# Kernel tuning notes

Measured on AMD Instinct MI355X. Metric: run time of the kernel, lower is better.

The kernel has to match this reference:

```python
import jax, jax.numpy as jnp
import numpy as np

H = 3072; NH = 24; HD = 128; MLP_D = 12288
B = 1; IMG = 1536; REF = 512; TXT = 256

def _gelu_tanh(x):
    return jax.nn.gelu(x, approximate=True)

def _ln(x, eps=1e-6):
    m = jnp.mean(x, axis=-1, keepdims=True)
    v = jnp.var(x, axis=-1, keepdims=True)
    return (x - m) * jax.lax.rsqrt(v + eps)

def _rms(x, g, eps=1e-6):
    return x * jax.lax.rsqrt(jnp.mean(x * x, axis=-1, keepdims=True) + eps) * g

def _rot_half(x):
    # interleaved rotate-half: (x0,x1,x2,x3,...) -> (-x1,x0,-x3,x2,...)
    x2 = x.reshape(x.shape[:-1] + (-1, 2))
    return jnp.stack([-x2[..., 1], x2[..., 0]], axis=-1).reshape(x.shape)

def setup_inputs():
    key = jax.random.key(0)
    ks = jax.random.split(key, 16)
    s = 0.02
    # rope tables for image tokens (interleaved layout, values repeated x2)
    inv_freq = 1.0 / (10000.0 ** (jnp.arange(0, HD // 2, dtype=jnp.float32) / (HD // 2)))
    ang = jnp.arange(IMG, dtype=jnp.float32)[:, None] * inv_freq[None, :]   # [IMG, HD//2]
    ang = jnp.repeat(ang, 2, axis=-1)                                       # [IMG, HD]
    return {
        'x':   jax.random.normal(ks[0], (B, IMG + TXT, H), jnp.float32),
        'vec': jax.random.normal(ks[1], (B, H), jnp.float32),
        'ref': jax.random.normal(ks[2], (B, REF, H), jnp.float32),
        'cos': jnp.cos(ang), 'sin': jnp.sin(ang),
        'mod_w':  jax.random.normal(ks[3], (H, 3 * H), jnp.float32) * s,
        'mod_b':  jnp.zeros((3 * H,), jnp.float32),
        'rf1_w':  jax.random.normal(ks[4], (H, H), jnp.float32) * s,
        'rf1_b':  jnp.zeros((H,), jnp.float32),
        'rf2_w':  jax.random.normal(ks[5], (H, H), jnp.float32) * s,
        'rf2_b':  jnp.zeros((H,), jnp.float32),
        'rln_g':  jnp.ones((H,), jnp.float32),
        'rln_b':  jnp.zeros((H,), jnp.float32),
        'lin1_w': jax.random.normal(ks[6], (H, 3 * H + MLP_D), jnp.float32) * s,
        'lin1_b': jnp.zeros((3 * H + MLP_D,), jnp.float32),
        'q_g':    jnp.ones((HD,), jnp.float32),
        'k_g':    jnp.ones((HD,), jnp.float32),
        'lin2_w': jax.random.normal(ks[7], (H + MLP_D, H), jnp.float32) * s,
        'lin2_b': jnp.zeros((H,), jnp.float32),
        'text_mask': jnp.ones((B, TXT), jnp.int32),
        'img_len': IMG, 'txt_len': TXT,
    }

def _forward(x, vec, ref, cos, sin, mod_w, mod_b, rf1_w, rf1_b, rf2_w, rf2_b,
             rln_g, rln_b, lin1_w, lin1_b, q_g, k_g, lin2_w, lin2_b,
             text_mask, img_len, txt_len):
    Bb = x.shape[0]
    ref_len = ref.shape[1]
    # modulation (ModulateDiT: SiLU -> Linear -> chunk(3))
    mod = jnp.dot(jax.nn.silu(vec), mod_w) + mod_b
    shift, scale, gate = jnp.split(mod, 3, axis=-1)
    x_mod = _ln(x) * (1.0 + scale[:, None]) + shift[:, None]
    # ref MLP + affine LayerNorm
    r = jnp.dot(_gelu_tanh(jnp.dot(ref, rf1_w) + rf1_b), rf2_w) + rf2_b
    r = _ln(r) * rln_g + rln_b
    # token reassembly: [img | ref | txt]
    xc = jnp.concatenate([x_mod[:, :img_len], r, x_mod[:, img_len:]], axis=1)
    h = jnp.dot(xc, lin1_w) + lin1_b
    qkv, mlp = h[..., :3 * H], h[..., 3 * H:]
    L2 = xc.shape[1]
    q, k, v = [t.reshape(Bb, L2, NH, HD) for t in jnp.split(qkv, 3, axis=-1)]
    # q drops the ref span; ref contributes K/V only
    q = jnp.concatenate([q[:, :img_len], q[:, img_len + ref_len:]], axis=1)
    q = _rms(q, q_g)
    k = _rms(k, k_g)
    # rotary only on image tokens
    c = cos[None, :, None, :]; s = sin[None, :, None, :]
    img_q = q[:, :img_len] * c + _rot_half(q[:, :img_len]) * s
    img_k = k[:, :img_len] * c + _rot_half(k[:, :img_len]) * s
    q = jnp.concatenate([img_q, q[:, img_len:]], axis=1)          # [B, Lq, NH, HD]
    k = jnp.concatenate([img_k, k[:, img_len:]], axis=1)          # [B, Lkv, NH, HD]
    # varlen mask (cu_seqlens semantics): valid attends valid, pad attends pad
    tmask = text_mask.astype(bool)
    qv  = jnp.concatenate([jnp.ones((Bb, img_len), bool), tmask], axis=1)
    kvv = jnp.concatenate([jnp.ones((Bb, img_len + ref_len), bool), tmask], axis=1)
    allowed = (qv[:, None, :, None] == kvv[:, None, None, :])     # [B,1,Lq,Lkv]
    scores = jnp.einsum('bqhd,bkhd->bhqk', q, k) * (HD ** -0.5)
    scores = jnp.where(allowed, scores, jnp.asarray(-1e9, scores.dtype))
    p = jax.nn.softmax(scores, axis=-1)
    attn = jnp.einsum('bhqk,bkhd->bqhd', p, v).reshape(Bb, img_len + txt_len, H)
    mlp = jnp.concatenate([mlp[:, :img_len], mlp[:, img_len + ref_len:]], axis=1)
    out = jnp.dot(jnp.concatenate([attn, _gelu_tanh(mlp)], axis=-1), lin2_w) + lin2_b
    return x + out * gate[:, None]

def reference(x, vec, ref, cos, sin, mod_w, mod_b, rf1_w, rf1_b, rf2_w, rf2_b,
              rln_g, rln_b, lin1_w, lin1_b, q_g, k_g, lin2_w, lin2_b,
              text_mask, img_len, txt_len):
    return _forward(x, vec, ref, cos, sin, mod_w, mod_b, rf1_w, rf1_b, rf2_w, rf2_b,
                    rln_g, rln_b, lin1_w, lin1_b, q_g, k_g, lin2_w, lin2_b,
                    text_mask, img_len, txt_len)
```

## Files before the change

kernel.cpp:

```cpp
#include <hip/hip_runtime.h>
#include <cstdint>
#include <cstddef>

typedef unsigned short u16;
typedef unsigned int   u32;
typedef __bf16 bf16_t;
typedef bf16_t bf16x8 __attribute__((ext_vector_type(8)));
typedef float  f32x4  __attribute__((ext_vector_type(4)));
typedef u16    u16x4  __attribute__((ext_vector_type(4)));


__device__ __forceinline__ float b2f(u16 b){ u32 u=((u32)b)<<16; float f; __builtin_memcpy(&f,&u,4); return f; }
__device__ __forceinline__ u16 f2b(float f){ u32 u; __builtin_memcpy(&u,&f,4); u = u + 0x7fffu + ((u>>16)&1u); return (u16)(u>>16); }
__device__ __forceinline__ float gelu_f(float x){
  float x3 = x*x*x;
  return 0.5f*x*(1.f + tanhf(0.7978845608028654f*(x + 0.044715f*x3)));
}

__device__ __forceinline__ void gload_lds16(const void* g, void* l){
  __builtin_amdgcn_global_load_lds((const __attribute__((address_space(1))) void*)g,
                                   (__attribute__((address_space(3))) void*)l, 16, 0, 0);
}

template<int NW, bool MX>
__device__ __forceinline__ float bred(float v, float* red){
  #pragma unroll
  for (int o=32;o;o>>=1){ float u=__shfl_down(v,o,64); v = MX? fmaxf(v,u) : v+u; }
  const int t = threadIdx.x;
  if ((t&63)==0) red[t>>6]=v;
  __syncthreads();
  float r = red[0];
  #pragma unroll
  for (int i=1;i<NW;i++) r = MX? fmaxf(r,red[i]) : r+red[i];
  __syncthreads();
  return r;
}

__device__ __forceinline__ void unpack8(uint4 u, float* f){
  f[0]=b2f((u16)(u.x&0xffffu)); f[1]=b2f((u16)(u.x>>16));
  f[2]=b2f((u16)(u.y&0xffffu)); f[3]=b2f((u16)(u.y>>16));
  f[4]=b2f((u16)(u.z&0xffffu)); f[5]=b2f((u16)(u.z>>16));
  f[6]=b2f((u16)(u.w&0xffffu)); f[7]=b2f((u16)(u.w>>16));
}

__global__ void modv_part(const float* __restrict__ vec, const float* __restrict__ W,
                          float* __restrict__ part){
  __shared__ float s[128];
  const int t = threadIdx.x;
  const int j = blockIdx.x*256 + t;
  const int i0 = blockIdx.y*128;
  if (t < 128){ float v = vec[i0+t]; s[t] = v/(1.f+__expf(-v)); }
  __syncthreads();
  float acc = 0.f;
  #pragma unroll 8
  for (int i=0;i<128;i++) acc += s[i]*W[(size_t)(i0+i)*9216 + j];
  part[(size_t)blockIdx.y*9216 + j] = acc;
}
__global__ void modv_reduce(const float* __restrict__ part, const float* __restrict__ mb,
                            float* __restrict__ modp){
  const int j = blockIdx.x*256 + threadIdx.x;
  float a = mb[j];
  #pragma unroll
  for (int c=0;c<24;c++) a += part[(size_t)c*9216 + j];
  modp[j] = a;
}

__global__ void convT(const float* __restrict__ W, u16* __restrict__ Wt, int Kd, int Nd){
  __shared__ float Ls[32][33];
  const int tx = threadIdx.x, ty = threadIdx.y;
  const int n0 = blockIdx.x*32, k0 = blockIdx.y*32;
  #pragma unroll
  for (int r=0;r<4;r++) Ls[ty+r*8][tx] = W[(size_t)(k0+ty+r*8)*Nd + n0+tx];
  __syncthreads();
  #pragma unroll
  for (int r=0;r<4;r++) Wt[(size_t)(n0+ty+r*8)*Kd + k0+tx] = f2b(Ls[tx][ty+r*8]);
}

__global__ void convertF2B(const float* __restrict__ src, u16* __restrict__ dst){
  const size_t i = ((size_t)blockIdx.x*256 + threadIdx.x)*4;
  const float4 v = *(const float4*)(src+i);
  u16x4 o; o.x=f2b(v.x); o.y=f2b(v.y); o.z=f2b(v.z); o.w=f2b(v.w);
  *(u16x4*)(dst+i) = o;
}

__global__ void ln_modulate(const float* __restrict__ x, const float* __restrict__ modp,
                            u16* __restrict__ xc){
  __shared__ float red[4];
  const int row = blockIdx.x, t = threadIdx.x;
  const float* xr = x + (size_t)row*3072;
  float4 v[3]; float s=0.f, ss=0.f;
  #pragma unroll
  for (int k=0;k<3;k++){
    v[k] = *(const float4*)(xr + t*4 + k*1024);
    s  += v[k].x+v[k].y+v[k].z+v[k].w;
    ss += v[k].x*v[k].x+v[k].y*v[k].y+v[k].z*v[k].z+v[k].w*v[k].w;
  }
  s  = bred<4,false>(s, red);
  ss = bred<4,false>(ss, red);
  const float mean = s*(1.f/3072.f);
  const float inv = rsqrtf(ss*(1.f/3072.f)-mean*mean + 1e-6f);
  const int orow = row<1536 ? row : row+512;
  u16* o = xc + (size_t)orow*3072;
  const float* shiftp = modp; const float* scalep = modp+3072;
  #pragma unroll
  for (int k=0;k<3;k++){
    const int j = t*4 + k*1024;
    const float4 sc = *(const float4*)(scalep+j);
    const float4 sh = *(const float4*)(shiftp+j);
    u16x4 ov;
    ov.x = f2b((v[k].x-mean)*inv*(1.f+sc.x)+sh.x);
    ov.y = f2b((v[k].y-mean)*inv*(1.f+sc.y)+sh.y);
    ov.z = f2b((v[k].z-mean)*inv*(1.f+sc.z)+sh.z);
    ov.w = f2b((v[k].w-mean)*inv*(1.f+sc.w)+sh.w);
    *(u16x4*)(o+j) = ov;
  }
}

__global__ void ln_ref(const float* __restrict__ rt, const float* __restrict__ g,
                       const float* __restrict__ b, u16* __restrict__ xc){
  __shared__ float red[4];
  const int row = blockIdx.x, t = threadIdx.x;
  const float* xr = rt + (size_t)row*3072;
  float4 v[3]; float s=0.f, ss=0.f;
  #pragma unroll
  for (int k=0;k<3;k++){
    v[k] = *(const float4*)(xr + t*4 + k*1024);
    s  += v[k].x+v[k].y+v[k].z+v[k].w;
    ss += v[k].x*v[k].x+v[k].y*v[k].y+v[k].z*v[k].z+v[k].w*v[k].w;
  }
  s  = bred<4,false>(s, red);
  ss = bred<4,false>(ss, red);
  const float mean = s*(1.f/3072.f);
  const float inv = rsqrtf(ss*(1.f/3072.f)-mean*mean + 1e-6f);
  u16* o = xc + (size_t)(1536+row)*3072;
  #pragma unroll
  for (int k=0;k<3;k++){
    const int j = t*4 + k*1024;
    const float4 gv = *(const float4*)(g+j);
    const float4 bv = *(const float4*)(b+j);
    u16x4 ov;
    ov.x = f2b((v[k].x-mean)*inv*gv.x+bv.x);
    ov.y = f2b((v[k].y-mean)*inv*gv.y+bv.y);
    ov.z = f2b((v[k].z-mean)*inv*gv.z+bv.z);
    ov.w = f2b((v[k].w-mean)*inv*gv.w+bv.w);
    *(u16x4*)(o+j) = ov;
  }
}

__global__ void qk_prep(const u16* __restrict__ h, const float* __restrict__ qg,
                        const float* __restrict__ kg, const float* __restrict__ cosb,
                        const float* __restrict__ sinb, u16* __restrict__ Q,
                        u16* __restrict__ Kb){
  __shared__ float red[4];
  const int row = blockIdx.x, hd = blockIdx.y, d = threadIdx.x;
  const u16* hr = h + (size_t)row*21504;
  const float kv = b2f(hr[3072 + hd*128 + d]);
  const bool doq = (row < 1536) || (row >= 2048);
  const float qv = doq ? b2f(hr[hd*128 + d]) : 0.f;
  float a = kv*kv, b = qv*qv;
  #pragma unroll
  for (int o=32;o;o>>=1){ a += __shfl_down(a,o,64); b += __shfl_down(b,o,64); }
  if ((d&63)==0){ red[(d>>6)*2] = a; red[(d>>6)*2+1] = b; }
  __syncthreads();
  const float kinv = rsqrtf((red[0]+red[2])*(1.f/128.f) + 1e-6f);
  const float qinv = rsqrtf((red[1]+red[3])*(1.f/128.f) + 1e-6f);
  float kn = kv*kinv*kg[d];
  float qn = qv*qinv*qg[d];
  if (row < 1536){
    const float c  = cosb[row*128 + d];
    const float sn = sinb[row*128 + d];
    const float ko = b2f(hr[3072 + hd*128 + (d^1)])*kinv*kg[d^1];
    const float qo = b2f(hr[hd*128 + (d^1)])*qinv*qg[d^1];
    const float krh = (d&1) ? ko : -ko;
    const float qrh = (d&1) ? qo : -qo;
    kn = kn*c + krh*sn;
    qn = qn*c + qrh*sn;
  }
  Kb[((size_t)hd*2304 + row)*128 + d] = f2b(kn);
  if (doq){
    const int qrow = row<1536 ? row : row-512;
    Q[((size_t)hd*1792 + qrow)*128 + d] = f2b(qn);
  }
}

__global__ void v_transpose(const u16* __restrict__ h, u16* __restrict__ VT){
  __shared__ u16 Ls[32][33];
  const int tx = threadIdx.x, ty = threadIdx.y;
  const int l0 = blockIdx.x*32, d0 = blockIdx.y*32, hd = blockIdx.z;
  #pragma unroll
  for (int r=0;r<4;r++)
    Ls[ty+r*8][tx] = h[(size_t)(l0+ty+r*8)*21504 + 6144 + hd*128 + d0 + tx];
  __syncthreads();
  #pragma unroll
  for (int r=0;r<4;r++)
    VT[((size_t)hd*128 + d0+ty+r*8)*2304 + l0 + tx] = Ls[tx][ty+r*8];
}

template<int EPI>
__global__ __launch_bounds__(256)
void gemm_bt(const u16* __restrict__ A, const u16* __restrict__ Bt,
             const float* __restrict__ bias, void* __restrict__ Cv,
             int K, int ldA, int ldB, int ldC,
             long long sA, long long sB, long long sC)
{
  __shared__ u16 As[128*32];
  __shared__ u16 Bs[128*32];
  const int t = threadIdx.x;
  const int w = t>>6, lane = t&63;
  const int bm = blockIdx.y, bn = blockIdx.x, bz = blockIdx.z;
  const u16* Ab = A + (size_t)((long long)bz*sA) + (size_t)bm*128*ldA;
  const u16* Bb = Bt + (size_t)((long long)bz*sB) + (size_t)bn*128*ldB;
  const int wm = w>>1, wn = w&1;
  const int lr = lane&15, lk = lane>>4;
  const int row0 = t>>2, kp0 = (t&3)*8;
  char* AsB = (char*)As; char* BsB = (char*)Bs;
  const int off0 = w*1024;
  const int off1 = 4096 + w*1024;
  f32x4 acc[4][4] = {};

  for (int kt = 0; kt < K; kt += 32){
    __syncthreads();
    gload_lds16(Ab + (size_t)row0*ldA + kt + kp0,      AsB + off0);
    gload_lds16(Ab + (size_t)(row0+64)*ldA + kt + kp0, AsB + off1);
    gload_lds16(Bb + (size_t)row0*ldB + kt + kp0,      BsB + off0);
    gload_lds16(Bb + (size_t)(row0+64)*ldB + kt + kp0, BsB + off1);
    __syncthreads();
    bf16x8 av[4], bv[4];
    #pragma unroll
    for (int i=0;i<4;i++) av[i] = *(const bf16x8*)(As + (wm*64+i*16+lr)*32 + lk*8);
    #pragma unroll
    for (int j=0;j<4;j++) bv[j] = *(const bf16x8*)(Bs + (wn*64+j*16+lr)*32 + lk*8);
    #pragma unroll
    for (int i=0;i<4;i++)
      #pragma unroll
      for (int j=0;j<4;j++)
        acc[i][j] = __builtin_amdgcn_mfma_f32_16x16x32_bf16(av[i], bv[j], acc[i][j], 0,0,0);
  }

  const int mBase = bm*128 + wm*64;
  const int nBase = bn*128 + wn*64;
  #pragma unroll
  for (int i=0;i<4;i++){
    #pragma unroll
    for (int j=0;j<4;j++){
      #pragma unroll
      for (int r=0;r<4;r++){
        const int m = mBase + i*16 + lk*4 + r;
        const int n = nBase + j*16 + lr;
        const float v = acc[i][j][r];
        const long long idx = (long long)bz*sC + (long long)m*ldC + n;
        if (EPI==6){
          ((float*)Cv)[idx] = v;
        } else {
          ((u16*)Cv)[idx] = f2b(v + bias[n]);
        }
      }
    }
  }
}

__global__ void comb_gelu(const float* __restrict__ P, const float* __restrict__ b,
                          u16* __restrict__ o){
  const size_t e = ((size_t)blockIdx.x*256 + threadIdx.x)*4;
  const int n = (int)(e % 3072);
  const size_t S = (size_t)512*3072;
  float4 a = *(const float4*)(P + e);
  #pragma unroll
  for (int c=1;c<6;c++){
    const float4 p = *(const float4*)(P + c*S + e);
    a.x+=p.x; a.y+=p.y; a.z+=p.z; a.w+=p.w;
  }
  const float4 bb = *(const float4*)(b + n);
  u16x4 ov;
  ov.x = f2b(gelu_f(a.x+bb.x)); ov.y = f2b(gelu_f(a.y+bb.y));
  ov.z = f2b(gelu_f(a.z+bb.z)); ov.w = f2b(gelu_f(a.w+bb.w));
  *(u16x4*)(o + e) = ov;
}
__global__ void comb_bias(const float* __restrict__ P, const float* __restrict__ b,
                          float* __restrict__ o){
  const size_t e = ((size_t)blockIdx.x*256 + threadIdx.x)*4;
  const int n = (int)(e % 3072);
  const size_t S = (size_t)512*3072;
  float4 a = *(const float4*)(P + e);
  #pragma unroll
  for (int c=1;c<6;c++){
    const float4 p = *(const float4*)(P + c*S + e);
    a.x+=p.x; a.y+=p.y; a.z+=p.z; a.w+=p.w;
  }
  const float4 bb = *(const float4*)(b + n);
  float4 ov; ov.x=a.x+bb.x; ov.y=a.y+bb.y; ov.z=a.z+bb.z; ov.w=a.w+bb.w;
  *(float4*)(o + e) = ov;
}

#define G256_BAR()  asm volatile("s_barrier" ::: "memory")

template<int CEPI>
__global__ __launch_bounds__(512,2)
void gemm256(const u16* __restrict__ A, const u16* __restrict__ Bt,
             const float* __restrict__ bias, void* __restrict__ Cv, void* __restrict__ Cv2,
             int Kc, int ld, int ldC, int nbn, int ntile, long long sC, int nwg, int gm)
{
  __shared__ char smem[131072];
  const int t = threadIdx.x;
  const int wid = t>>6, lane = t&63;
  const int lr = lane&15, lk = lane>>4;
  const int wm = wid>>2, wn = wid&3;

  const int orig = blockIdx.x;
  const int q8 = nwg>>3, r8 = nwg&7;
  const int xcd = orig&7, jj = orig>>3;
  const int wg = (xcd<r8 ? xcd*(q8+1) : r8*(q8+1) + (xcd-r8)*q8) + jj;
  int sk, bm, bn;
  if (gm > 0){
    const int band = wg / (gm*nbn);
    const int rr = wg - band*(gm*nbn);
    bn = rr / gm;
    bm = band*gm + (rr - bn*gm);
    sk = 0;
  } else {
    sk = wg / ntile;
    const int rem = wg - sk*ntile;
    bm = rem / nbn; bn = rem % nbn;
  }

  const u16* Agl = A  + (size_t)bm*256*ld + (size_t)sk*Kc;
  const u16* Bgl = Bt + (size_t)bn*256*ld + (size_t)sk*Kc;
  const int NT = Kc>>6;

  const int d0 = wid*64 + lane;
  const int sr = d0>>3;
  const size_t soff = (size_t)sr*ld + (size_t)(((d0&7)^(sr&7))<<3);

  const int xsl0 = ((lk    ) ^ (lr&7))<<4;
  const int xsl1 = ((lk | 4) ^ (lr&7))<<4;

  f32x4 acc[8][4] = {};
  bf16x8 bv[4][2];

  auto STAGE = [&](const u16* g, int h, int kt, char* ldsMat){
    const u16* s0 = g + (size_t)(h*128)*ld + kt + soff;
    char* l0 = ldsMat + h*16384 + wid*1024;
    gload_lds16(s0, l0);
    gload_lds16(s0 + (size_t)64*ld, l0 + 8192);
  };

  STAGE(Agl, 0, 0, smem);
  STAGE(Agl, 1, 0, smem);
  STAGE(Bgl, 0, 0, smem + 32768);
  STAGE(Bgl, 1, 0, smem + 32768);
  if (NT > 1){
    STAGE(Bgl, 0, 64, smem + 65536 + 32768);
    STAGE(Bgl, 1, 64, smem + 65536 + 32768);
    asm volatile("s_waitcnt vmcnt(4)" ::: "memory");
  } else {
    asm volatile("s_waitcnt vmcnt(0)" ::: "memory");
  }
  G256_BAR();

#define G256_MFMA_Q(Q)                                                          \
  do{                                                                           \
    _Pragma("unroll")                                                           \
    for (int j=0;j<4;j++){                                                      \
      acc[(Q)*2+0][j] = __builtin_amdgcn_mfma_f32_16x16x32_bf16(av00, bv[j][0], acc[(Q)*2+0][j], 0,0,0); \
      acc[(Q)*2+0][j] = __builtin_amdgcn_mfma_f32_16x16x32_bf16(av01, bv[j][1], acc[(Q)*2+0][j], 0,0,0); \
      acc[(Q)*2+1][j] = __builtin_amdgcn_mfma_f32_16x16x32_bf16(av10, bv[j][0], acc[(Q)*2+1][j], 0,0,0); \
      acc[(Q)*2+1][j] = __builtin_amdgcn_mfma_f32_16x16x32_bf16(av11, bv[j][1], acc[(Q)*2+1][j], 0,0,0); \
    }                                                                           \
  }while(0)

#define G256_PHASE(Q, STG, TAILW)                                               \
  do{                                                                           \
    const char* abase = cA + (wm*128 + (Q)*32 + lr)*128;                        \
    bf16x8 av00 = *(const bf16x8*)(abase + xsl0);                               \
    bf16x8 av01 = *(const bf16x8*)(abase + xsl1);                               \
    bf16x8 av10 = *(const bf16x8*)(abase + 2048 + xsl0);                        \
    bf16x8 av11 = *(const bf16x8*)(abase + 2048 + xsl1);                        \
    if ((Q)==0){                                                                \
      _Pragma("unroll")                                                         \
      for (int j=0;j<4;j++){                                                    \
        const char* bbase = cB + (wn*64 + j*16 + lr)*128;                       \
        bv[j][0] = *(const bf16x8*)(bbase + xsl0);                              \
        bv[j][1] = *(const bf16x8*)(bbase + xsl1);                              \
      }                                                                         \
    }                                                                           \
    STG;                                                                        \
    G256_BAR();                                                                 \
    __builtin_amdgcn_s_setprio(1);                                              \
    G256_MFMA_Q(Q);                                                             \
    __builtin_amdgcn_s_setprio(0);                                              \
    TAILW;                                                                      \
    G256_BAR();                                                                 \
  }while(0)

  for (int tt = 0; tt < NT; ++tt){
    char* cA = smem + (tt&1)*65536;
    char* cB = cA + 32768;
    char* nA = smem + ((tt+1)&1)*65536;
    const int kt1 = (tt+1)<<6, kt2 = (tt+2)<<6;
    const bool stA = (tt+1) < NT, stB = (tt+2) < NT;

    G256_PHASE(0, if (stA) STAGE(Agl, 0, kt1, nA), );
    G256_PHASE(1, if (stA) STAGE(Agl, 1, kt1, nA), );
    G256_PHASE(2, if (stB) STAGE(Bgl, 0, kt2, cB), );
    G256_PHASE(3, if (stB) STAGE(Bgl, 1, kt2, cB),
               if (stB)      { asm volatile("s_waitcnt vmcnt(4)" ::: "memory"); }
               else if (stA) { asm volatile("s_waitcnt vmcnt(0)" ::: "memory"); } );
  }
#undef G256_PHASE
#undef G256_MFMA_Q

  const int mB = bm*256 + wm*128 + lk*4;
  const int nB = bn*256 + wn*64 + lr;
  #pragma unroll
  for (int fi=0; fi<8; fi++){
    #pragma unroll
    for (int j=0; j<4; j++){
      const int n = nB + j*16;
      const float bb = (CEPI==2) ? bias[n] : 0.f;
      #pragma unroll
      for (int r=0;r<4;r++){
        const int m = mB + fi*16 + r;
        if (CEPI==1){
          ((float*)Cv)[(size_t)sk*sC + (size_t)m*ldC + n] = acc[fi][j][r];
        } else {
          if (n < 9216){
            ((u16*)Cv)[(size_t)m*ldC + n] = f2b(acc[fi][j][r] + bb);
          } else {
            const int qm = (m < 1536) ? m : (m >= 2048 ? m - 512 : -1);
            if (qm >= 0)
              ((u16*)Cv2)[(size_t)qm*15360 + 3072 + (n - 9216)] = f2b(gelu_f(acc[fi][j][r] + bb));
          }
        }
      }
    }
  }
}

__global__ __launch_bounds__(512)
void flash_attn(const u16* __restrict__ Qb, const u16* __restrict__ Kb,
                const u16* __restrict__ VT, const int* __restrict__ tmask,
                u16* __restrict__ out2)
{
  __shared__ __attribute__((aligned(16))) char smf[114688];
  char* Qs  = smf;
  char* Ks0 = smf + 32768;
  char* Vs0 = smf + 65536;
  char* Ps  = smf + 98304;
  const int t = threadIdx.x, wid = t>>6, lane = t&63;
  const int lr = lane&15, hi = lane>>4;
  const int head = blockIdx.y, qt = blockIdx.x;
  const int q0 = qt*128;
  const u16* Qg = Qb + ((size_t)head*1792 + q0)*128;
  const u16* Kg = Kb + (size_t)head*2304*128;
  const u16* Vg = VT + (size_t)head*128*2304;
  const float SCALE = 0.08838834764831845f;

  u32 kbits = 0;
  #pragma unroll
  for (int i=0;i<16;i++) kbits |= (u32)(tmask[i*16 + lr] != 0) << i;
  int fqr[4];
  #pragma unroll
  for (int r=0;r<4;r++){
    const int q = q0 + wid*16 + hi*4 + r;
    fqr[r] = (q < 1536) ? 1 : (tmask[q-1536] != 0);
  }

  #pragma unroll
  for (int c=0;c<4;c++){
    const int s = c*512 + wid*64 + lane;
    const int row = s>>4, dsl = s&15;
    gload_lds16(Qg + (size_t)row*128 + ((dsl ^ (row&7))<<3),
                Qs + (size_t)(c*512 + wid*64)*16);
  }
  #pragma unroll
  for (int c=0;c<2;c++){
    const int s = c*512 + wid*64 + lane;
    { const int row = s>>4, dsl = s&15;
      gload_lds16(Kg + (size_t)row*128 + ((dsl ^ (row&7))<<3),
                  Ks0 + (size_t)(c*512 + wid*64)*16); }
    { const int row = s>>3, dsl = s&7;
      gload_lds16(Vg + (size_t)row*2304 + ((dsl ^ (row&7))<<3),
                  Vs0 + (size_t)(c*512 + wid*64)*16); }
  }
  asm volatile("s_waitcnt vmcnt(0)" ::: "memory");
  __syncthreads();

  bf16x8 av[4];
  {
    const int row = wid*16 + lr;
    #pragma unroll
    for (int ks=0;ks<4;ks++)
      av[ks] = *(const bf16x8*)(Qs + row*256 + (((ks*4+hi) ^ (row&7))<<4));
  }

  f32x4 acc[8] = {};
  float m_[4], l_[4];
  #pragma unroll
  for (int r=0;r<4;r++){ m_[r] = -3e38f; l_[r] = 0.f; }

  for (int kt = 0; kt < 36; ++kt){
    char* Kc = Ks0 + (kt&1)*16384;
    char* Vc = Vs0 + (kt&1)*16384;
    if (kt+1 < 36){
      char* Kn = Ks0 + ((kt+1)&1)*16384;
      char* Vn = Vs0 + ((kt+1)&1)*16384;
      #pragma unroll
      for (int c=0;c<2;c++){
        const int s = c*512 + wid*64 + lane;
        { const int row = s>>4, dsl = s&15;
          gload_lds16(Kg + (size_t)((kt+1)*64 + row)*128 + ((dsl ^ (row&7))<<3),
                      Kn + (size_t)(c*512 + wid*64)*16); }
        { const int row = s>>3, dsl = s&7;
          gload_lds16(Vg + (size_t)row*2304 + (kt+1)*64 + ((dsl ^ (row&7))<<3),
                      Vn + (size_t)(c*512 + wid*64)*16); }
      }
    }
    f32x4 sacc[4] = {};
    #pragma unroll
    for (int ks=0;ks<4;ks++){
      #pragma unroll
      for (int j=0;j<4;j++){
        const int row = j*16 + lr;
        bf16x8 bk = *(const bf16x8*)(Kc + row*256 + (((ks*4+hi) ^ (row&7))<<4));
        sacc[j] = __builtin_amdgcn_mfma_f32_16x16x32_bf16(av[ks], bk, sacc[j], 0,0,0);
      }
    }
    int gkj[4];
    #pragma unroll
    for (int j=0;j<4;j++)
      gkj[j] = (kt < 32) ? 1 : (int)((kbits >> ((kt-32)*4 + j)) & 1u);
    float p[4][4]; bool alw[4][4];
    float mt[4] = {-3e38f,-3e38f,-3e38f,-3e38f};
    #pragma unroll
    for (int j=0;j<4;j++){
      #pragma unroll
      for (int r=0;r<4;r++){
        const float s = sacc[j][r]*SCALE;
        const bool a = (fqr[r] == gkj[j]);
        alw[j][r] = a; p[j][r] = s;
        if (a) mt[r] = fmaxf(mt[r], s);
      }
    }
    #pragma unroll
    for (int r=0;r<4;r++){
      #pragma unroll
      for (int o=1;o<16;o<<=1) mt[r] = fmaxf(mt[r], __shfl_xor(mt[r], o, 64));
      const float nm = fmaxf(m_[r], mt[r]);
      const float cr = __expf(m_[r] - nm);
      m_[r] = nm;
      l_[r] *= cr;
      #pragma unroll
      for (int jp=0;jp<8;jp++) acc[jp][r] *= cr;
    }
    float rs[4] = {0.f,0.f,0.f,0.f};
    #pragma unroll
    for (int j=0;j<4;j++){
      #pragma unroll
      for (int r=0;r<4;r++){
        const float pv = alw[j][r] ? __expf(p[j][r] - m_[r]) : 0.f;
        p[j][r] = pv; rs[r] += pv;
      }
    }
    #pragma unroll
    for (int r=0;r<4;r++){
      #pragma unroll
      for (int o=1;o<16;o<<=1) rs[r] += __shfl_xor(rs[r], o, 64);
      l_[r] += rs[r];
    }
    #pragma unroll
    for (int j=0;j<4;j++){
      #pragma unroll
      for (int r=0;r<4;r++){
        const int q = wid*16 + hi*4 + r;
        const int k = j*16 + lr;
        *(u16*)(Ps + q*128 + (((k>>3) ^ (q&7))<<4) + (k&7)*2) = f2b(p[j][r]);
      }
    }
    asm volatile("s_waitcnt lgkmcnt(0)" ::: "memory");
    __builtin_amdgcn_sched_barrier(0);
    bf16x8 pa[2];
    {
      const int row = wid*16 + lr;
      #pragma unroll
      for (int ks2=0;ks2<2;ks2++)
        pa[ks2] = *(const bf16x8*)(Ps + row*128 + (((ks2*4+hi) ^ (row&7))<<4));
    }
    #pragma unroll
    for (int ks2=0;ks2<2;ks2++){
      #pragma unroll
      for (int jp=0;jp<8;jp++){
        const int row = jp*16 + lr;
        bf16x8 bvv = *(const bf16x8*)(Vc + row*128 + (((ks2*4+hi) ^ (row&7))<<4));
        acc[jp] = __builtin_amdgcn_mfma_f32_16x16x32_bf16(pa[ks2], bvv, acc[jp], 0,0,0);
      }
    }
    asm volatile("s_waitcnt vmcnt(0)" ::: "memory");
    __syncthreads();
  }

  float inv[4];
  #pragma unroll
  for (int r=0;r<4;r++) inv[r] = 1.f/l_[r];
  #pragma unroll
  for (int jp=0;jp<8;jp++){
    #pragma unroll
    for (int r=0;r<4;r++){
      const size_t q = q0 + wid*16 + hi*4 + r;
      out2[q*15360 + head*128 + jp*16 + lr] = f2b(acc[jp][r]*inv[r]);
    }
  }
}

__global__ void lin2_fin(const float* __restrict__ P, const float* __restrict__ x,
                         const float* __restrict__ bias, const float* __restrict__ gate,
                         float* __restrict__ out){
  const size_t e = ((size_t)blockIdx.x*256 + threadIdx.x)*4;
  const int n = (int)(e % 3072);
  const size_t S = (size_t)1792*3072;
  const float4 p0 = *(const float4*)(P + e);
  const float4 p1 = *(const float4*)(P + S + e);
  const float4 p2 = *(const float4*)(P + 2*S + e);
  const float4 bb = *(const float4*)(bias + n);
  const float4 gg = *(const float4*)(gate + n);
  const float4 xv = *(const float4*)(x + e);
  float4 o;
  o.x = xv.x + (p0.x+p1.x+p2.x+bb.x)*gg.x;
  o.y = xv.y + (p0.y+p1.y+p2.y+bb.y)*gg.y;
  o.z = xv.z + (p0.z+p1.z+p2.z+bb.z)*gg.z;
  o.w = xv.w + (p0.w+p1.w+p2.w+bb.w)*gg.w;
  *(float4*)(out + e) = o;
}

extern "C" void kernel_launch(void* const* d_in, const int* in_sizes, int n_in,
                              void* d_out, int out_size, void* d_ws, size_t ws_size,
                              hipStream_t stream)
{
  (void)in_sizes; (void)n_in; (void)out_size; (void)ws_size;
  const float* x     = (const float*)d_in[0];
  const float* vec   = (const float*)d_in[1];
  const float* ref   = (const float*)d_in[2];
  const float* cosb  = (const float*)d_in[3];
  const float* sinb  = (const float*)d_in[4];
  const float* mod_w = (const float*)d_in[5];
  const float* mod_b = (const float*)d_in[6];
  const float* rf1_w = (const float*)d_in[7];
  const float* rf1_b = (const float*)d_in[8];
  const float* rf2_w = (const float*)d_in[9];
  const float* rf2_b = (const float*)d_in[10];
  const float* rln_g = (const float*)d_in[11];
  const float* rln_b = (const float*)d_in[12];
  const float* lin1_w= (const float*)d_in[13];
  const float* lin1_b= (const float*)d_in[14];
  const float* q_g   = (const float*)d_in[15];
  const float* k_g   = (const float*)d_in[16];
  const float* lin2_w= (const float*)d_in[17];
  const float* lin2_b= (const float*)d_in[18];
  const int*   tmask = (const int*)d_in[19];
  float* out = (float*)d_out;
  char* ws = (char*)d_ws;

  float* modp = (float*)(ws + 0);
  float* part = (float*)(ws + 36864);
  u16*  w2t   = (u16*)(ws + 921600);
  u16*  Qb    = (u16*)(ws + 95293440ll);
  u16*  Kb    = (u16*)(ws + 106303488ll);
  u16*  VT    = (u16*)(ws + 120459264ll);
  u16*  out2  = (u16*)(ws + 134615040ll);
  u16*  w1t   = (u16*)(ws + 189665280ll);
  u16*  xc    = (u16*)(ws + 321785856ll);
  u16*  rf1t  = (u16*)(ws + 335941632ll);
  u16*  rf2t  = (u16*)(ws + 354816000ll);
  u16*  refb  = (u16*)(ws + 373690368ll);
  u16*  tb    = (u16*)(ws + 376836096ll);
  float* rtmp = (float*)(ws + 379981824ll);
  float* rp   = (float*)(ws + 386273280ll);
  u16*  hbuf  = (u16*)(ws + 335941632ll);
  float* p2b  = (float*)(ws + 189665280ll);

  modv_part<<<dim3(36,24),256,0,stream>>>(vec, mod_w, part);
  modv_reduce<<<36,256,0,stream>>>(part, mod_b, modp);
  convT<<<dim3(96,96), dim3(32,8),0,stream>>>(rf1_w, rf1t, 3072, 3072);
  convT<<<dim3(96,96), dim3(32,8),0,stream>>>(rf2_w, rf2t, 3072, 3072);
  convT<<<dim3(672,96),dim3(32,8),0,stream>>>(lin1_w, w1t, 3072, 21504);
  convT<<<dim3(96,480),dim3(32,8),0,stream>>>(lin2_w, w2t, 15360, 3072);
  convertF2B<<<1536,256,0,stream>>>(ref, refb);
  ln_modulate<<<1792,256,0,stream>>>(x, modp, xc);
  gemm_bt<6><<<dim3(24,4,6),256,0,stream>>>(refb, rf1t, nullptr, rp, 512, 3072,3072,3072,
                                            512,512, (long long)512*3072);
  comb_gelu<<<1536,256,0,stream>>>(rp, rf1_b, tb);
  gemm_bt<6><<<dim3(24,4,6),256,0,stream>>>(tb, rf2t, nullptr, rp, 512, 3072,3072,3072,
                                            512,512, (long long)512*3072);
  comb_bias<<<1536,256,0,stream>>>(rp, rf2_b, rtmp);
  ln_ref<<<512,256,0,stream>>>(rtmp, rln_g, rln_b, xc);
  gemm256<2><<<756,512,0,stream>>>(xc, w1t, lin1_b, hbuf, out2, 3072, 3072, 21504, 84, 756, 0, 756, 3);
  qk_prep<<<dim3(2304,24),128,0,stream>>>(hbuf, q_g, k_g, cosb, sinb, Qb, Kb);
  v_transpose<<<dim3(72,4,24),dim3(32,8),0,stream>>>(hbuf, VT);
  flash_attn<<<dim3(14,24),512,0,stream>>>(Qb, Kb, VT, tmask, out2);
  gemm256<1><<<252,512,0,stream>>>(out2, w2t, nullptr, p2b, nullptr, 5120, 15360, 3072, 12, 84,
                                   (long long)1792*3072, 252, 0);
  lin2_fin<<<5376,256,0,stream>>>(p2b, x, lin2_b, modp + 6144, out);
}
```

Before: 964.4 us.

## Widen weight transpose tiles, use exp-based GELU, add LDS wait before MFMA

The weight transpose-and-convert kernel now uses 64x64 tiles, with float4 global reads and 8-byte bf16 writes, so fewer blocks are launched and memory accesses are wider. GELU tanh is rewritten algebraically as x*sigmoid(2u) using __expf, which is cheaper than tanhf but slightly less accurate. The big GEMM now uses the builtin barrier plus an explicit lgkmcnt(0) wait and sched_barrier before the MFMA phase. That wait fixes LDS read ordering but may stop the compiler from overlapping LDS reads with MFMAs. The unused unpack8 helper is removed.

```diff
diff --git a/kernel.cpp b/kernel.cpp
--- a/kernel.cpp
+++ b/kernel.cpp
@@ -13,8 +13,8 @@
 __device__ __forceinline__ float b2f(u16 b){ u32 u=((u32)b)<<16; float f; __builtin_memcpy(&f,&u,4); return f; }
 __device__ __forceinline__ u16 f2b(float f){ u32 u; __builtin_memcpy(&u,&f,4); u = u + 0x7fffu + ((u>>16)&1u); return (u16)(u>>16); }
 __device__ __forceinline__ float gelu_f(float x){
-  float x3 = x*x*x;
-  return 0.5f*x*(1.f + tanhf(0.7978845608028654f*(x + 0.044715f*x3)));
+  const float u2 = 1.5957691216057308f*(x + 0.044715f*x*x*x);
+  return x/(1.f + __expf(-u2));
 }
 
 __device__ __forceinline__ void gload_lds16(const void* g, void* l){
@@ -34,13 +34,6 @@
   for (int i=1;i<NW;i++) r = MX? fmaxf(r,red[i]) : r+red[i];
   __syncthreads();
   return r;
-}
-
-__device__ __forceinline__ void unpack8(uint4 u, float* f){
-  f[0]=b2f((u16)(u.x&0xffffu)); f[1]=b2f((u16)(u.x>>16));
-  f[2]=b2f((u16)(u.y&0xffffu)); f[3]=b2f((u16)(u.y>>16));
-  f[4]=b2f((u16)(u.z&0xffffu)); f[5]=b2f((u16)(u.z>>16));
-  f[6]=b2f((u16)(u.w&0xffffu)); f[7]=b2f((u16)(u.w>>16));
 }
 
 __global__ void modv_part(const float* __restrict__ vec, const float* __restrict__ W,
@@ -65,15 +58,28 @@
   modp[j] = a;
 }
 
-__global__ void convT(const float* __restrict__ W, u16* __restrict__ Wt, int Kd, int Nd){
-  __shared__ float Ls[32][33];
-  const int tx = threadIdx.x, ty = threadIdx.y;
-  const int n0 = blockIdx.x*32, k0 = blockIdx.y*32;
-  #pragma unroll
-  for (int r=0;r<4;r++) Ls[ty+r*8][tx] = W[(size_t)(k0+ty+r*8)*Nd + n0+tx];
+__global__ __launch_bounds__(256)
+void convT(const float* __restrict__ W, u16* __restrict__ Wt, int Kd, int Nd){
+  __shared__ float Ls[64][65];
+  const int t = threadIdx.x;
+  const int n0 = blockIdx.x*64, k0 = blockIdx.y*64;
+  const int tr = t>>4;
+  const int tc = (t&15)*4;
+  #pragma unroll
+  for (int p=0;p<4;p++){
+    const int kk = tr + p*16;
+    const float4 v = *(const float4*)(W + (size_t)(k0+kk)*Nd + n0 + tc);
+    Ls[kk][tc+0]=v.x; Ls[kk][tc+1]=v.y; Ls[kk][tc+2]=v.z; Ls[kk][tc+3]=v.w;
+  }
   __syncthreads();
   #pragma unroll
-  for (int r=0;r<4;r++) Wt[(size_t)(n0+ty+r*8)*Kd + k0+tx] = f2b(Ls[tx][ty+r*8]);
+  for (int p=0;p<4;p++){
+    const int nn = tr + p*16;
+    u16x4 o;
+    o.x = f2b(Ls[tc+0][nn]); o.y = f2b(Ls[tc+1][nn]);
+    o.z = f2b(Ls[tc+2][nn]); o.w = f2b(Ls[tc+3][nn]);
+    *(u16x4*)(Wt + (size_t)(n0+nn)*Kd + k0 + tc) = o;
+  }
 }
 
 __global__ void convertF2B(const float* __restrict__ src, u16* __restrict__ dst){
@@ -292,7 +298,9 @@
   *(float4*)(o + e) = ov;
 }
 
-#define G256_BAR()  asm volatile("s_barrier" ::: "memory")
+#define G256_BAR()  __builtin_amdgcn_s_barrier()
+#define G256_LGKM() do{ asm volatile("s_waitcnt lgkmcnt(0)" ::: "memory"); \
+                        __builtin_amdgcn_sched_barrier(0); }while(0)
 
 template<int CEPI>
 __global__ __launch_bounds__(512,2)
@@ -385,6 +393,7 @@
     }                                                                           \
     STG;                                                                        \
     G256_BAR();                                                                 \
+    G256_LGKM();                                                                \
     __builtin_amdgcn_s_setprio(1);                                              \
     G256_MFMA_Q(Q);                                                             \
     __builtin_amdgcn_s_setprio(0);                                              \
@@ -679,10 +688,10 @@
 
   modv_part<<<dim3(36,24),256,0,stream>>>(vec, mod_w, part);
   modv_reduce<<<36,256,0,stream>>>(part, mod_b, modp);
-  convT<<<dim3(96,96), dim3(32,8),0,stream>>>(rf1_w, rf1t, 3072, 3072);
-  convT<<<dim3(96,96), dim3(32,8),0,stream>>>(rf2_w, rf2t, 3072, 3072);
-  convT<<<dim3(672,96),dim3(32,8),0,stream>>>(lin1_w, w1t, 3072, 21504);
-  convT<<<dim3(96,480),dim3(32,8),0,stream>>>(lin2_w, w2t, 15360, 3072);
+  convT<<<dim3(48,48),  256,0,stream>>>(rf1_w, rf1t, 3072, 3072);
+  convT<<<dim3(48,48),  256,0,stream>>>(rf2_w, rf2t, 3072, 3072);
+  convT<<<dim3(336,48), 256,0,stream>>>(lin1_w, w1t, 3072, 21504);
+  convT<<<dim3(48,240), 256,0,stream>>>(lin2_w, w2t, 15360, 3072);
   convertF2B<<<1536,256,0,stream>>>(ref, refb);
   ln_modulate<<<1792,256,0,stream>>>(x, modp, xc);
   gemm_bt<6><<<dim3(24,4,6),256,0,stream>>>(refb, rf1t, nullptr, rp, 512, 3072,3072,3072,
```

After: 935.8 us. 3.0% less time.
